# Kernel tuning notes

Hardware: AMD Instinct MI355X
Metric: run time of the kernel (lower is better)

The kernel has to match this reference:

```python
import jax, jax.numpy as jnp
import numpy as np

NUM_CLASSES = 80
M = 50.0  # MAX_ANOT_ANCHOR_POSITION_DISTANCE
ALPHA = 0.25
GAMMA = 2.0
EPS = 1e-4


def setup_inputs() -> dict:
    key = jax.random.key(0)
    k1, k2, k3, k4, k5 = jax.random.split(key, 5)
    B, N, C, K = 8, 100000, NUM_CLASSES, 32
    classifications = jax.random.uniform(k1, (B, N, C), dtype=jnp.float32,
                                         minval=0.01, maxval=0.99)
    regressions = jax.random.normal(k2, (B, N, 3), dtype=jnp.float32)
    # anchors: x,y in [0,1000), alpha in [0, 2*pi)
    axy = jax.random.uniform(k3, (1, N, 2), dtype=jnp.float32) * 1000.0
    aal = jax.random.uniform(k3, (1, N, 1), dtype=jnp.float32) * 6.2831853
    anchors = jnp.concatenate([axy, aal], axis=-1)
    gxy = jax.random.uniform(k4, (B, K, 2), dtype=jnp.float32) * 1000.0
    gal = jax.random.uniform(k4, (B, K, 1), dtype=jnp.float32) * 6.2831853
    lab = jax.random.randint(k5, (B, K, 1), 0, C).astype(jnp.float32)
    annotations = jnp.concatenate([gxy, gal, lab], axis=-1)
    return {"classifications": classifications, "regressions": regressions,
            "anchors": anchors, "annotations": annotations}


def _per_image(cls_p, reg, anchor, ann):
    # cls_p: [N,C], reg: [N,3], anchor: [N,3], ann: [K,4]
    C = cls_p.shape[1]
    cls_p = jnp.clip(cls_p, EPS, 1.0 - EPS)
    # distance [N,K] = 10*sqrt(dx^2+dy^2) + |dalpha|
    dx = anchor[:, 0:1] - ann[None, :, 0]
    dy = anchor[:, 1:2] - ann[None, :, 1]
    da = jnp.abs(anchor[:, 2:3] - ann[None, :, 2])
    dist = 10.0 * jnp.sqrt(dx * dx + dy * dy) + da
    dmin = jnp.min(dist, axis=1)          # [N]
    amin = jnp.argmin(dist, axis=1)       # [N]
    pos = dmin <= 11.0 * M                # [N]
    neg = dmin >= 13.0 * M                # [N]
    assigned = ann[amin]                  # [N,4]
    labels = assigned[:, 3].astype(jnp.int32)
    onehot = jax.nn.one_hot(labels, C, dtype=jnp.bool_)
    targets = jnp.where((neg | pos)[:, None], 0.0, -1.0)   # [N,C]
    targets = jnp.where(pos[:, None] & onehot, 1.0, targets)
    is_pos_t = targets == 1.0
    alpha_f = jnp.where(is_pos_t, ALPHA, 1.0 - ALPHA)
    focal_w = alpha_f * jnp.where(is_pos_t, 1.0 - cls_p, cls_p) ** GAMMA
    bce = -(targets * jnp.log(cls_p) + (1.0 - targets) * jnp.log(1.0 - cls_p))
    cls_loss = jnp.where(targets != -1.0, focal_w * bce, 0.0)
    num_pos = jnp.sum(pos.astype(jnp.float32))
    cls_l = jnp.sum(cls_loss) / jnp.maximum(num_pos, 1.0)
    tgt = assigned[:, :3] - anchor                     # [N,3]
    diff_xy = jnp.abs(tgt[:, :2] - reg[:, :2])         # [N,2]
    diff_ang = 1.0 - jnp.cos(tgt[:, 2] - reg[:, 2])    # [N]
    lxy = jnp.where(diff_xy <= 1.0 / 9.0,
                    0.5 * 9.0 * diff_xy * diff_xy,
                    diff_xy - 0.5 / 9.0)
    posf = pos.astype(jnp.float32)
    denom = jnp.maximum(num_pos, 1.0)
    reg_l = jnp.sum(lxy * posf[:, None]) / (2.0 * denom) \
          + jnp.sum(diff_ang * posf) / denom
    reg_l = jnp.where(num_pos > 0, reg_l, 0.0)
    return cls_l, reg_l


def reference(classifications, regressions, anchors, annotations):
    anchor = anchors[0]  # [N,3]
    cls_ls, reg_ls = jax.vmap(_per_image, in_axes=(0, 0, None, 0))(
        classifications, regressions, anchor, annotations)
    return (jnp.mean(cls_ls, keepdims=True), jnp.mean(reg_ls, keepdims=True))
```

## Files before the change

### kernel.cpp

```cpp
#include <hip/hip_runtime.h>

#define NUM_CLASSES 80
#define K_ANN 32
#define NF4 (NUM_CLASSES / 4)
#define TILE 256
#define ITER (TILE * NF4 / 256)
#define UNROLL 4
#define PREF 4

typedef float f32x4 __attribute__((ext_vector_type(4)));


__global__ __launch_bounds__(256, 8) void focal_main(
    const float* __restrict__ cls,
    const float* __restrict__ reg,
    const float* __restrict__ anc,
    const float* __restrict__ ann,
    float* __restrict__ ws,
    int N, int nblk)
{
    const int b  = blockIdx.y;
    const int bx = blockIdx.x;
    const int t  = threadIdx.x;
    const int n0 = bx * TILE;
    const bool full = (n0 + TILE <= N);

    __shared__ f32x4  s_pref[PREF * 256];
    __shared__ float4 s_ann4[K_ANN];
    __shared__ float  s_g[TILE];

    if (t < K_ANN)
        s_ann4[t] = ((const float4*)(ann + (long long)b * K_ANN * 4))[t];

    const f32x4* __restrict__ base =
        (const f32x4*)(cls + ((long long)b * N + n0) * NUM_CLASSES);

    if (full) {
        const int wid = t >> 6;
        #pragma unroll
        for (int u = 0; u < PREF; ++u)
            __builtin_amdgcn_global_load_lds(
                (const __attribute__((address_space(1))) unsigned int*)&base[u * 256 + t],
                (__attribute__((address_space(3))) unsigned int*)&s_pref[u * 256 + wid * 64],
                16, 0, 0);
    }
    __syncthreads();

    float csum = 0.f, npos = 0.f, rxy = 0.f, rang = 0.f;

    {
        const int n = n0 + t;
        const bool ok = n < N;
        const int m = ok ? n : N - 1;
        const float ax = anc[m * 3 + 0], ay = anc[m * 3 + 1], aa = anc[m * 3 + 2];
        const float r0 = reg[((long long)b * N + m) * 3 + 0];
        const float r1 = reg[((long long)b * N + m) * 3 + 1];
        const float r2 = reg[((long long)b * N + m) * 3 + 2];

        float d1 = 1e30f;
        int   k1 = 0;
        #pragma unroll 4
        for (int k = 0; k < K_ANN; ++k) {
            const float4 a4 = s_ann4[k];
            const float dx = ax - a4.x, dy = ay - a4.y;
            const float da = fabsf(aa - a4.z);
            const float d  = fmaf(10.f, sqrtf(fmaf(dx, dx, dy * dy)), da);
            if (d < d1) { d1 = d; k1 = k; }
        }

        const bool pos = ok && (d1 <= 550.f);
        const bool neg = ok && (d1 >= 650.f);
        s_g[t] = (pos | neg) ? 0.75f : 0.f;

        if (pos) {
            const float4 a4 = s_ann4[k1];
            const float tx = a4.x - ax, ty = a4.y - ay, tz = a4.z - aa;
            const float dxr = fabsf(tx - r0);
            const float dyr = fabsf(ty - r1);
            rxy += ((dxr <= 1.f / 9.f) ? 4.5f * dxr * dxr : dxr - 0.5f / 9.f)
                 + ((dyr <= 1.f / 9.f) ? 4.5f * dyr * dyr : dyr - 0.5f / 9.f);
            rang += 1.f - __cosf(tz - r2);
            npos += 1.f;

            const int lab = (int)a4.w;
            const float p = cls[((long long)b * N + n) * NUM_CLASSES + lab];
            csum += 0.75f * p * p * __logf(1.f - p)
                  - 0.25f * (1.f - p) * (1.f - p) * __logf(p);
        }
    }
    __syncthreads();

    float acc = 0.f;
    if (full) {
        #pragma unroll
        for (int u = 0; u < PREF; ++u) {
            const unsigned idx = (unsigned)(u * 256 + t);
            const float g = s_g[idx / 20u];
            const f32x4 v = s_pref[idx];
            float s4 = 0.f;
            s4 = fmaf(v.x * v.x, __logf(1.f - v.x), s4);
            s4 = fmaf(v.y * v.y, __logf(1.f - v.y), s4);
            s4 = fmaf(v.z * v.z, __logf(1.f - v.z), s4);
            s4 = fmaf(v.w * v.w, __logf(1.f - v.w), s4);
            acc = fmaf(g, s4, acc);
        }
        #pragma unroll 1
        for (int i0 = PREF; i0 < ITER; i0 += UNROLL) {
            unsigned ix[UNROLL];
            float    g [UNROLL];
            f32x4    v [UNROLL];
            #pragma unroll
            for (int u = 0; u < UNROLL; ++u) {
                ix[u] = (unsigned)((i0 + u) * 256 + t);
                g[u]  = s_g[ix[u] / 20u];
            }
            #pragma unroll
            for (int u = 0; u < UNROLL; ++u)
                v[u] = base[(g[u] != 0.f) ? ix[u] : (unsigned)t];
            __builtin_amdgcn_sched_barrier(0);
            #pragma unroll
            for (int u = 0; u < UNROLL; ++u) {
                float s4 = 0.f;
                s4 = fmaf(v[u].x * v[u].x, __logf(1.f - v[u].x), s4);
                s4 = fmaf(v[u].y * v[u].y, __logf(1.f - v[u].y), s4);
                s4 = fmaf(v[u].z * v[u].z, __logf(1.f - v[u].z), s4);
                s4 = fmaf(v[u].w * v[u].w, __logf(1.f - v[u].w), s4);
                acc = fmaf(g[u], s4, acc);
            }
        }
    } else {
        const int total4 = (N - n0) * NF4;
        for (int i = t; i < total4; i += 256) {
            const float g = s_g[(unsigned)i / 20u];
            const f32x4 v = base[(g != 0.f) ? i : t];
            float s4 = 0.f;
            s4 = fmaf(v.x * v.x, __logf(1.f - v.x), s4);
            s4 = fmaf(v.y * v.y, __logf(1.f - v.y), s4);
            s4 = fmaf(v.z * v.z, __logf(1.f - v.z), s4);
            s4 = fmaf(v.w * v.w, __logf(1.f - v.w), s4);
            acc = fmaf(g, s4, acc);
        }
    }
    csum -= acc;

    #pragma unroll
    for (int off = 32; off > 0; off >>= 1) {
        csum += __shfl_down(csum, off);
        npos += __shfl_down(npos, off);
        rxy  += __shfl_down(rxy , off);
        rang += __shfl_down(rang, off);
    }
    __shared__ float s_red[4][4];
    const int wid = t >> 6;
    if ((t & 63) == 0) {
        s_red[wid][0] = csum; s_red[wid][1] = npos;
        s_red[wid][2] = rxy;  s_red[wid][3] = rang;
    }
    __syncthreads();
    if (t == 0) {
        float a0 = 0.f, a1 = 0.f, a2 = 0.f, a3 = 0.f;
        #pragma unroll
        for (int w = 0; w < 4; ++w) {
            a0 += s_red[w][0]; a1 += s_red[w][1];
            a2 += s_red[w][2]; a3 += s_red[w][3];
        }
        float4* slot = (float4*)(ws + ((long long)b * nblk + bx) * 4);
        *slot = make_float4(a0, a1, a2, a3);
    }
}

__global__ __launch_bounds__(512) void focal_final(
    const float* __restrict__ ws, float* __restrict__ out, int B, int nblk)
{
    const int t    = threadIdx.x;
    const int b    = t >> 6;
    const int lane = t & 63;

    float a0 = 0.f, a1 = 0.f, a2 = 0.f, a3 = 0.f;
    if (b < B) {
        for (int i = lane; i < nblk; i += 64) {
            const float4 v = *(const float4*)(ws + ((long long)b * nblk + i) * 4);
            a0 += v.x; a1 += v.y; a2 += v.z; a3 += v.w;
        }
    }
    #pragma unroll
    for (int off = 32; off > 0; off >>= 1) {
        a0 += __shfl_down(a0, off);
        a1 += __shfl_down(a1, off);
        a2 += __shfl_down(a2, off);
        a3 += __shfl_down(a3, off);
    }

    __shared__ float s_cl[8], s_rl[8];
    if (lane == 0 && b < B) {
        const float den = fmaxf(a1, 1.f);
        s_cl[b] = a0 / den;
        const float r = a2 / (2.f * den) + a3 / den;
        s_rl[b] = (a1 > 0.f) ? r : 0.f;
    }
    __syncthreads();
    if (t == 0) {
        float cl = 0.f, rl = 0.f;
        for (int i = 0; i < B; ++i) { cl += s_cl[i]; rl += s_rl[i]; }
        out[0] = cl / (float)B;
        out[1] = rl / (float)B;
    }
}

extern "C" void kernel_launch(void* const* d_in, const int* in_sizes, int n_in,
                              void* d_out, int out_size, void* d_ws, size_t ws_size,
                              hipStream_t stream)
{
    (void)n_in; (void)out_size; (void)ws_size;
    const float* cls = (const float*)d_in[0];
    const float* reg = (const float*)d_in[1];
    const float* anc = (const float*)d_in[2];
    const float* ann = (const float*)d_in[3];
    float* out = (float*)d_out;
    float* ws  = (float*)d_ws;

    const int N = in_sizes[2] / 3;
    const int B = in_sizes[3] / (K_ANN * 4);
    const int nblk = (N + TILE - 1) / TILE;

    dim3 grid(nblk, B);
    focal_main<<<grid, dim3(256), 0, stream>>>(cls, reg, anc, ann, ws, N, nblk);
    focal_final<<<1, dim3(512), 0, stream>>>(ws, out, B, nblk);
}
```

Measured before the change: 57.80 us.

## Fuse final reduction via last-block atomic counter and reorder per-wave tile layout

Removes the separate finalize kernel by having the last block (detected by an atomic counter in workspace, zeroed by a memset) perform the cross-block reduction. Anchor, regression and annotation loads are hoisted ahead of the LDS prefetch, and the barrier after the prefetch waits only on LDS counters. The positive-label probability is loaded early but its log computation is deferred until after the main loop to overlap latency. Each wave now streams a contiguous chunk of the tile instead of interleaved slices. The change adds a memset launch and atomic traffic in exchange for dropping a kernel launch.

```diff
diff --git a/kernel.cpp b/kernel.cpp
--- a/kernel.cpp
+++ b/kernel.cpp
@@ -4,9 +4,9 @@
 #define K_ANN 32
 #define NF4 (NUM_CLASSES / 4)
 #define TILE 256
-#define ITER (TILE * NF4 / 256)
+#define WF4  (64 * NF4)
+#define PREFC 4
 #define UNROLL 4
-#define PREF 4
 
 typedef float f32x4 __attribute__((ext_vector_type(4)));
 
@@ -17,46 +17,60 @@
     const float* __restrict__ anc,
     const float* __restrict__ ann,
     float* __restrict__ ws,
+    float* __restrict__ out,
     int N, int nblk)
 {
-    const int b  = blockIdx.y;
-    const int bx = blockIdx.x;
-    const int t  = threadIdx.x;
-    const int n0 = bx * TILE;
+    const int b    = blockIdx.y;
+    const int bx   = blockIdx.x;
+    const int t    = threadIdx.x;
+    const int wid  = t >> 6;
+    const int lane = t & 63;
+    const int n0   = bx * TILE;
     const bool full = (n0 + TILE <= N);
 
-    __shared__ f32x4  s_pref[PREF * 256];
+    __shared__ f32x4  s_pref[4 * 256];
     __shared__ float4 s_ann4[K_ANN];
     __shared__ float  s_g[TILE];
-
-    if (t < K_ANN)
-        s_ann4[t] = ((const float4*)(ann + (long long)b * K_ANN * 4))[t];
+    __shared__ float  s_red[4][4];
+    __shared__ int    s_last;
+    __shared__ float  s_cl[16], s_rl[16];
 
     const f32x4* __restrict__ base =
         (const f32x4*)(cls + ((long long)b * N + n0) * NUM_CLASSES);
 
+    const int n  = n0 + t;
+    const bool ok = n < N;
+    const int m  = ok ? n : N - 1;
+    const float ax = anc[m * 3 + 0], ay = anc[m * 3 + 1], aa = anc[m * 3 + 2];
+    const float r0 = reg[((long long)b * N + m) * 3 + 0];
+    const float r1 = reg[((long long)b * N + m) * 3 + 1];
+    const float r2 = reg[((long long)b * N + m) * 3 + 2];
+    float4 annv = make_float4(0.f, 0.f, 0.f, 0.f);
+    if (t < K_ANN)
+        annv = ((const float4*)(ann + (long long)b * K_ANN * 4))[t];
+    __builtin_amdgcn_sched_barrier(0);
+
     if (full) {
-        const int wid = t >> 6;
+        const int rb = wid * WF4;
         #pragma unroll
-        for (int u = 0; u < PREF; ++u)
+        for (int c = 0; c < PREFC; ++c)
             __builtin_amdgcn_global_load_lds(
-                (const __attribute__((address_space(1))) unsigned int*)&base[u * 256 + t],
-                (__attribute__((address_space(3))) unsigned int*)&s_pref[u * 256 + wid * 64],
+                (const __attribute__((address_space(1))) unsigned int*)&base[rb + c * 64 + lane],
+                (__attribute__((address_space(3))) unsigned int*)&s_pref[wid * 256 + c * 64],
                 16, 0, 0);
     }
-    __syncthreads();
+
+    if (t < K_ANN) s_ann4[t] = annv;
+
+    asm volatile("s_waitcnt lgkmcnt(0)" ::: "memory");
+    __builtin_amdgcn_s_barrier();
+    asm volatile("" ::: "memory");
 
     float csum = 0.f, npos = 0.f, rxy = 0.f, rang = 0.f;
+    float pp = 0.f;
+    bool  do_p = false;
 
     {
-        const int n = n0 + t;
-        const bool ok = n < N;
-        const int m = ok ? n : N - 1;
-        const float ax = anc[m * 3 + 0], ay = anc[m * 3 + 1], aa = anc[m * 3 + 2];
-        const float r0 = reg[((long long)b * N + m) * 3 + 0];
-        const float r1 = reg[((long long)b * N + m) * 3 + 1];
-        const float r2 = reg[((long long)b * N + m) * 3 + 2];
-
         float d1 = 1e30f;
         int   k1 = 0;
         #pragma unroll 4
@@ -81,22 +95,21 @@
                  + ((dyr <= 1.f / 9.f) ? 4.5f * dyr * dyr : dyr - 0.5f / 9.f);
             rang += 1.f - __cosf(tz - r2);
             npos += 1.f;
-
             const int lab = (int)a4.w;
-            const float p = cls[((long long)b * N + n) * NUM_CLASSES + lab];
-            csum += 0.75f * p * p * __logf(1.f - p)
-                  - 0.25f * (1.f - p) * (1.f - p) * __logf(p);
+            pp = cls[((long long)b * N + n) * NUM_CLASSES + lab];
+            do_p = true;
         }
     }
     __syncthreads();
 
     float acc = 0.f;
     if (full) {
+        const int rb = wid * WF4;
         #pragma unroll
-        for (int u = 0; u < PREF; ++u) {
-            const unsigned idx = (unsigned)(u * 256 + t);
-            const float g = s_g[idx / 20u];
-            const f32x4 v = s_pref[idx];
+        for (int c = 0; c < PREFC; ++c) {
+            const int idx = rb + c * 64 + lane;
+            const float g = s_g[(unsigned)idx / 20u];
+            const f32x4 v = s_pref[wid * 256 + c * 64 + lane];
             float s4 = 0.f;
             s4 = fmaf(v.x * v.x, __logf(1.f - v.x), s4);
             s4 = fmaf(v.y * v.y, __logf(1.f - v.y), s4);
@@ -105,18 +118,17 @@
             acc = fmaf(g, s4, acc);
         }
         #pragma unroll 1
-        for (int i0 = PREF; i0 < ITER; i0 += UNROLL) {
-            unsigned ix[UNROLL];
-            float    g [UNROLL];
-            f32x4    v [UNROLL];
+        for (int c0 = PREFC; c0 < NF4; c0 += UNROLL) {
+            float g[UNROLL];
+            f32x4 v[UNROLL];
+            #pragma unroll
+            for (int u = 0; u < UNROLL; ++u)
+                g[u] = s_g[(unsigned)(rb + (c0 + u) * 64 + lane) / 20u];
             #pragma unroll
             for (int u = 0; u < UNROLL; ++u) {
-                ix[u] = (unsigned)((i0 + u) * 256 + t);
-                g[u]  = s_g[ix[u] / 20u];
-            }
-            #pragma unroll
-            for (int u = 0; u < UNROLL; ++u)
-                v[u] = base[(g[u] != 0.f) ? ix[u] : (unsigned)t];
+                const int idx = rb + (c0 + u) * 64 + lane;
+                v[u] = base[(g[u] != 0.f) ? idx : (rb + lane)];
+            }
             __builtin_amdgcn_sched_barrier(0);
             #pragma unroll
             for (int u = 0; u < UNROLL; ++u) {
@@ -142,6 +154,9 @@
         }
     }
     csum -= acc;
+    if (do_p)
+        csum += 0.75f * pp * pp * __logf(1.f - pp)
+              - 0.25f * (1.f - pp) * (1.f - pp) * __logf(pp);
 
     #pragma unroll
     for (int off = 32; off > 0; off >>= 1) {
@@ -150,9 +165,7 @@
         rxy  += __shfl_down(rxy , off);
         rang += __shfl_down(rang, off);
     }
-    __shared__ float s_red[4][4];
-    const int wid = t >> 6;
-    if ((t & 63) == 0) {
+    if (lane == 0) {
         s_red[wid][0] = csum; s_red[wid][1] = npos;
         s_red[wid][2] = rxy;  s_red[wid][3] = rang;
     }
@@ -166,44 +179,43 @@
         }
         float4* slot = (float4*)(ws + ((long long)b * nblk + bx) * 4);
         *slot = make_float4(a0, a1, a2, a3);
-    }
-}
-
-__global__ __launch_bounds__(512) void focal_final(
-    const float* __restrict__ ws, float* __restrict__ out, int B, int nblk)
-{
-    const int t    = threadIdx.x;
-    const int b    = t >> 6;
-    const int lane = t & 63;
-
-    float a0 = 0.f, a1 = 0.f, a2 = 0.f, a3 = 0.f;
-    if (b < B) {
-        for (int i = lane; i < nblk; i += 64) {
-            const float4 v = *(const float4*)(ws + ((long long)b * nblk + i) * 4);
-            a0 += v.x; a1 += v.y; a2 += v.z; a3 += v.w;
-        }
-    }
-    #pragma unroll
-    for (int off = 32; off > 0; off >>= 1) {
-        a0 += __shfl_down(a0, off);
-        a1 += __shfl_down(a1, off);
-        a2 += __shfl_down(a2, off);
-        a3 += __shfl_down(a3, off);
-    }
-
-    __shared__ float s_cl[8], s_rl[8];
-    if (lane == 0 && b < B) {
-        const float den = fmaxf(a1, 1.f);
-        s_cl[b] = a0 / den;
-        const float r = a2 / (2.f * den) + a3 / den;
-        s_rl[b] = (a1 > 0.f) ? r : 0.f;
+        __threadfence();
+        unsigned* cnt = (unsigned*)(ws + (size_t)gridDim.y * nblk * 4);
+        const unsigned total = (unsigned)nblk * gridDim.y;
+        s_last = (atomicAdd(cnt, 1u) == total - 1u);
     }
     __syncthreads();
-    if (t == 0) {
-        float cl = 0.f, rl = 0.f;
-        for (int i = 0; i < B; ++i) { cl += s_cl[i]; rl += s_rl[i]; }
-        out[0] = cl / (float)B;
-        out[1] = rl / (float)B;
+
+    if (s_last) {
+        __threadfence();
+        const int B = (int)gridDim.y;
+        for (int bb = wid; bb < B; bb += 4) {
+            float a0 = 0.f, a1 = 0.f, a2 = 0.f, a3 = 0.f;
+            for (int i = lane; i < nblk; i += 64) {
+                const float4 v = *(const float4*)(ws + ((long long)bb * nblk + i) * 4);
+                a0 += v.x; a1 += v.y; a2 += v.z; a3 += v.w;
+            }
+            #pragma unroll
+            for (int off = 32; off > 0; off >>= 1) {
+                a0 += __shfl_down(a0, off);
+                a1 += __shfl_down(a1, off);
+                a2 += __shfl_down(a2, off);
+                a3 += __shfl_down(a3, off);
+            }
+            if (lane == 0) {
+                const float den = fmaxf(a1, 1.f);
+                s_cl[bb] = a0 / den;
+                const float r = a2 / (2.f * den) + a3 / den;
+                s_rl[bb] = (a1 > 0.f) ? r : 0.f;
+            }
+        }
+        __syncthreads();
+        if (t == 0) {
+            float cl = 0.f, rl = 0.f;
+            for (int i = 0; i < B; ++i) { cl += s_cl[i]; rl += s_rl[i]; }
+            out[0] = cl / (float)B;
+            out[1] = rl / (float)B;
+        }
     }
 }
 
@@ -223,7 +235,8 @@
     const int B = in_sizes[3] / (K_ANN * 4);
     const int nblk = (N + TILE - 1) / TILE;
 
+    hipMemsetAsync((char*)d_ws + (size_t)B * nblk * 16, 0, 4, stream);
+
     dim3 grid(nblk, B);
-    focal_main<<<grid, dim3(256), 0, stream>>>(cls, reg, anc, ann, ws, N, nblk);
-    focal_final<<<1, dim3(512), 0, stream>>>(ws, out, B, nblk);
+    focal_main<<<grid, dim3(256), 0, stream>>>(cls, reg, anc, ann, ws, out, N, nblk);
 }
```

New measurement: 174.5 us. 3.02x slower.
